# Optimization experiments

Hardware: AMD Instinct MI355X
Metric: run time of the kernel (lower is better)

## Reference

```python
import jax, jax.numpy as jnp
import numpy as np

B, CIN, COUT, N = 64, 1024, 1024, 49   # batch, in_features, out_features, flattened spatial
GROUPS = 1
CHUNK = 16                              # output-channel tile to bound intermediate memory


def setup_inputs() -> dict:
    key = jax.random.key(0)
    k1, k2 = jax.random.split(key)
    x = jax.random.normal(k1, (B, CIN, N), dtype=jnp.float32)
    weight = jax.random.normal(k2, (COUT, CIN // GROUPS), dtype=jnp.float32)  # std=1.0 init
    bias = jnp.zeros((COUT,), dtype=jnp.float32)
    return {"x": x, "weight": weight, "bias": bias}


def norm_dist_inf(x, weight, groups, chunk):
    # x: [B, Cin, N], weight: [Cout, Cin//groups]
    # out[b, o, n] = max_d |x[b, g(o)*d + d', n] - weight[o, d']|  (L-inf distance)
    Bb, Cin, Nn = x.shape
    Cout, d = weight.shape
    og = Cout // groups
    xg = x.reshape(Bb, groups, d, Nn)                 # [B, g, d, N]
    wg = weight.reshape(groups, og, d)                # [g, og, d]
    # tile output channels to avoid materializing [B, Cout, Cin, N]
    wchunks = wg.reshape(groups, og // chunk, chunk, d).transpose(1, 0, 2, 3)  # [nc, g, chunk, d]

    def body(carry, wc):
        # diff: [B, g, chunk, d, N] -> max over d
        out = jnp.max(jnp.abs(xg[:, :, None, :, :] - wc[None, :, :, :, None]), axis=3)
        return carry, out                              # [B, g, chunk, N]

    _, outs = jax.lax.scan(body, None, wchunks)        # [nc, B, g, chunk, N]
    out = outs.transpose(1, 2, 0, 3, 4).reshape(Bb, Cout, Nn)
    return out


def reference(x, weight, bias):
    out = norm_dist_inf(x, weight, GROUPS, CHUNK)      # [B, Cout, N]
    return out + bias[None, :, None]
```

## Files before the change

### kernel.cpp

```cpp
#include <hip/hip_runtime.h>


typedef float v2f  __attribute__((ext_vector_type(2)));
typedef float v4sf __attribute__((ext_vector_type(4)));

constexpr int CIN  = 1024;
constexpr int COUT = 1024;
constexpr int NN   = 49;
constexpr int P    = 3136;
constexpr int CPW  = 8;
constexpr int PIX  = 2;
constexpr int PT   = 64 * PIX;
constexpr int NPT  = (P + PT - 1) / PT;
constexpr int NTL  = CIN / 4;

#define PKSUB(d, wp, xp) \
    asm("v_pk_add_f32 %0, %1, %2 neg_lo:[0,1] neg_hi:[0,1]" \
        : "=v"(d) : "s"(wp), "v"(xp))
#define AMAX3(a, lo, hi) \
    asm("v_max3_f32 %0, %0, |%1|, |%2|" : "+v"(a) : "v"(lo), "v"(hi))

#define ISSUE_W(buf, ptr) do {                                               \
    asm volatile("s_load_dwordx4 %0, %1, 0x0"    : "=s"(buf[0]) : "s"(ptr)); \
    asm volatile("s_load_dwordx4 %0, %1, 0x1000" : "=s"(buf[1]) : "s"(ptr)); \
    asm volatile("s_load_dwordx4 %0, %1, 0x2000" : "=s"(buf[2]) : "s"(ptr)); \
    asm volatile("s_load_dwordx4 %0, %1, 0x3000" : "=s"(buf[3]) : "s"(ptr)); \
    asm volatile("s_load_dwordx4 %0, %1, 0x4000" : "=s"(buf[4]) : "s"(ptr)); \
    asm volatile("s_load_dwordx4 %0, %1, 0x5000" : "=s"(buf[5]) : "s"(ptr)); \
    asm volatile("s_load_dwordx4 %0, %1, 0x6000" : "=s"(buf[6]) : "s"(ptr)); \
    asm volatile("s_load_dwordx4 %0, %1, 0x7000" : "=s"(buf[7]) : "s"(ptr)); \
} while (0)

#define SDRAIN() asm volatile("s_waitcnt lgkmcnt(0)" ::: "memory")

__global__ __launch_bounds__(64) void ndist_kernel(
    const float* __restrict__ x, const float* __restrict__ w,
    const float* __restrict__ bias, float* __restrict__ out)
{
    const int lane  = threadIdx.x;
    const int o0    = blockIdx.x * CPW;
    const int pbase = blockIdx.y * PT;

    int bb[PIX], nn_[PIX];
    const float* xp[PIX];
#pragma unroll
    for (int i = 0; i < PIX; ++i) {
        const bool valid = (pbase + i * 64) < P;
        const int  pi    = (valid ? pbase + i * 64 : pbase) + lane;
        bb[i]  = pi / NN;
        nn_[i] = pi - bb[i] * NN;
        xp[i]  = x + (size_t)bb[i] * (CIN * NN) + nn_[i];
    }

    const float* wb = w + (size_t)o0 * CIN;

    float acc[CPW][PIX];
#pragma unroll
    for (int c = 0; c < CPW; ++c)
#pragma unroll
        for (int i = 0; i < PIX; ++i) acc[c][i] = 0.0f;

    v2f  xA[PIX][2], xB[PIX][2];
    v4sf wS0[8], wS1[8];

#define LOAD_X(dst, kt) do {                                   \
        _Pragma("unroll")                                      \
        for (int i = 0; i < PIX; ++i) {                        \
            float a0 = xp[i][((kt) * 4 + 0) * NN];             \
            float a1 = xp[i][((kt) * 4 + 1) * NN];             \
            float a2 = xp[i][((kt) * 4 + 2) * NN];             \
            float a3 = xp[i][((kt) * 4 + 3) * NN];             \
            dst[i][0] = (v2f){a0, a1};                         \
            dst[i][1] = (v2f){a2, a3};                         \
        }                                                      \
    } while (0)

#define COMPUTE(xv, wbuf) do {                                 \
        _Pragma("unroll")                                      \
        for (int c = 0; c < CPW; ++c) {                        \
            v2f wlo = __builtin_shufflevector(wbuf[c], wbuf[c], 0, 1); \
            v2f whi = __builtin_shufflevector(wbuf[c], wbuf[c], 2, 3); \
            _Pragma("unroll")                                  \
            for (int i = 0; i < PIX; ++i) {                    \
                v2f d0, d1;                                    \
                PKSUB(d0, wlo, xv[i][0]);                      \
                PKSUB(d1, whi, xv[i][1]);                      \
                AMAX3(acc[c][i], d0.x, d0.y);                  \
                AMAX3(acc[c][i], d1.x, d1.y);                  \
            }                                                  \
        }                                                      \
    } while (0)

    ISSUE_W(wS0, wb);
    LOAD_X(xA, 0);
    SDRAIN();

    for (int kt = 0; kt < NTL - 2; kt += 2) {
        const float* w1 = wb + (size_t)(kt + 1) * 4;
        ISSUE_W(wS1, w1);
        LOAD_X(xB, kt + 1);
        COMPUTE(xA, wS0);
        SDRAIN();

        const float* w2 = wb + (size_t)(kt + 2) * 4;
        ISSUE_W(wS0, w2);
        LOAD_X(xA, kt + 2);
        COMPUTE(xB, wS1);
        SDRAIN();
    }
    {
        const float* w1 = wb + (size_t)(NTL - 1) * 4;
        ISSUE_W(wS1, w1);
        LOAD_X(xB, NTL - 1);
        COMPUTE(xA, wS0);
        SDRAIN();
        COMPUTE(xB, wS1);
    }

#pragma unroll
    for (int i = 0; i < PIX; ++i) {
        if ((pbase + i * 64) < P) {
#pragma unroll
            for (int c = 0; c < CPW; ++c) {
                const int o = o0 + c;
                out[((size_t)bb[i] * COUT + o) * NN + nn_[i]] = acc[c][i] + bias[o];
            }
        }
    }
}

extern "C" void kernel_launch(void* const* d_in, const int* in_sizes, int n_in,
                              void* d_out, int out_size, void* d_ws, size_t ws_size,
                              hipStream_t stream) {
    const float* x    = (const float*)d_in[0];
    const float* w    = (const float*)d_in[1];
    const float* bias = (const float*)d_in[2];
    float* out        = (float*)d_out;

    dim3 grid(COUT / CPW, NPT);
    ndist_kernel<<<grid, 64, 0, stream>>>(x, w, bias, out);
}
```

Baseline: 154.5 us.

## Pre-transpose x to channel-major workspace and load adjacent pixel pairs

```diff
diff --git a/kernel.cpp b/kernel.cpp
--- a/kernel.cpp
+++ b/kernel.cpp
@@ -9,16 +9,21 @@
 constexpr int NN   = 49;
 constexpr int P    = 3136;
 constexpr int CPW  = 8;
-constexpr int PIX  = 2;
-constexpr int PT   = 64 * PIX;
-constexpr int NPT  = (P + PT - 1) / PT;
+constexpr int PT   = 128;
+constexpr int NPT  = 25;
 constexpr int NTL  = CIN / 4;
 
+#define PKBC_LO(d, wp, xp) \
+    asm("v_pk_add_f32 %0, %1, %2 op_sel:[0,0] op_sel_hi:[0,1] neg_lo:[1,0] neg_hi:[1,0]" \
+        : "=v"(d) : "s"(wp), "v"(xp))
+#define PKBC_HI(d, wp, xp) \
+    asm("v_pk_add_f32 %0, %1, %2 op_sel:[1,0] op_sel_hi:[1,1] neg_lo:[1,0] neg_hi:[1,0]" \
+        : "=v"(d) : "s"(wp), "v"(xp))
+#define AMAX3(a, lo, hi) \
+    asm("v_max3_f32 %0, %0, |%1|, |%2|" : "+v"(a) : "v"(lo), "v"(hi))
 #define PKSUB(d, wp, xp) \
     asm("v_pk_add_f32 %0, %1, %2 neg_lo:[0,1] neg_hi:[0,1]" \
         : "=v"(d) : "s"(wp), "v"(xp))
-#define AMAX3(a, lo, hi) \
-    asm("v_max3_f32 %0, %0, |%1|, |%2|" : "+v"(a) : "v"(lo), "v"(hi))
 
 #define ISSUE_W(buf, ptr) do {                                               \
     asm volatile("s_load_dwordx4 %0, %1, 0x0"    : "=s"(buf[0]) : "s"(ptr)); \
@@ -30,64 +35,57 @@
     asm volatile("s_load_dwordx4 %0, %1, 0x6000" : "=s"(buf[6]) : "s"(ptr)); \
     asm volatile("s_load_dwordx4 %0, %1, 0x7000" : "=s"(buf[7]) : "s"(ptr)); \
 } while (0)
+#define SDRAIN() do { asm volatile("s_waitcnt lgkmcnt(0)" ::: "memory"); \
+                      __builtin_amdgcn_sched_barrier(0); } while (0)
 
-#define SDRAIN() asm volatile("s_waitcnt lgkmcnt(0)" ::: "memory")
+__global__ void transpose_x(const float* __restrict__ x, float* __restrict__ xT) {
+    const int pp = threadIdx.x & 63, kk = threadIdx.x >> 6;
+    const int p = blockIdx.x * 64 + pp;
+    const int k = blockIdx.y * 4 + kk;
+    const int b = p / NN, n = p - b * NN;
+    xT[(size_t)k * P + p] = x[(size_t)b * (CIN * NN) + (size_t)k * NN + n];
+}
 
 __global__ __launch_bounds__(64) void ndist_kernel(
-    const float* __restrict__ x, const float* __restrict__ w,
+    const float* __restrict__ xT, const float* __restrict__ w,
     const float* __restrict__ bias, float* __restrict__ out)
 {
     const int lane  = threadIdx.x;
     const int o0    = blockIdx.x * CPW;
     const int pbase = blockIdx.y * PT;
+    const int p0    = pbase + 2 * lane;
+    const int pc    = (p0 <= P - 2) ? p0 : (P - 2);
 
-    int bb[PIX], nn_[PIX];
-    const float* xp[PIX];
-#pragma unroll
-    for (int i = 0; i < PIX; ++i) {
-        const bool valid = (pbase + i * 64) < P;
-        const int  pi    = (valid ? pbase + i * 64 : pbase) + lane;
-        bb[i]  = pi / NN;
-        nn_[i] = pi - bb[i] * NN;
-        xp[i]  = x + (size_t)bb[i] * (CIN * NN) + nn_[i];
-    }
-
+    const float* __restrict__ xb = xT + pc;
     const float* wb = w + (size_t)o0 * CIN;
 
-    float acc[CPW][PIX];
+    float acc[CPW][2];
 #pragma unroll
-    for (int c = 0; c < CPW; ++c)
-#pragma unroll
-        for (int i = 0; i < PIX; ++i) acc[c][i] = 0.0f;
+    for (int c = 0; c < CPW; ++c) { acc[c][0] = 0.0f; acc[c][1] = 0.0f; }
 
-    v2f  xA[PIX][2], xB[PIX][2];
+    v2f  xA[4], xB[4];
     v4sf wS0[8], wS1[8];
 
 #define LOAD_X(dst, kt) do {                                   \
         _Pragma("unroll")                                      \
-        for (int i = 0; i < PIX; ++i) {                        \
-            float a0 = xp[i][((kt) * 4 + 0) * NN];             \
-            float a1 = xp[i][((kt) * 4 + 1) * NN];             \
-            float a2 = xp[i][((kt) * 4 + 2) * NN];             \
-            float a3 = xp[i][((kt) * 4 + 3) * NN];             \
-            dst[i][0] = (v2f){a0, a1};                         \
-            dst[i][1] = (v2f){a2, a3};                         \
-        }                                                      \
+        for (int j = 0; j < 4; ++j)                            \
+            dst[j] = *(const v2f*)(xb + (size_t)((kt) * 4 + j) * P); \
     } while (0)
 
 #define COMPUTE(xv, wbuf) do {                                 \
         _Pragma("unroll")                                      \
         for (int c = 0; c < CPW; ++c) {                        \
-            v2f wlo = __builtin_shufflevector(wbuf[c], wbuf[c], 0, 1); \
-            v2f whi = __builtin_shufflevector(wbuf[c], wbuf[c], 2, 3); \
-            _Pragma("unroll")                                  \
-            for (int i = 0; i < PIX; ++i) {                    \
-                v2f d0, d1;                                    \
-                PKSUB(d0, wlo, xv[i][0]);                      \
-                PKSUB(d1, whi, xv[i][1]);                      \
-                AMAX3(acc[c][i], d0.x, d0.y);                  \
-                AMAX3(acc[c][i], d1.x, d1.y);                  \
-            }                                                  \
+            v2f p01 = __builtin_shufflevector(wbuf[c], wbuf[c], 0, 1); \
+            v2f p23 = __builtin_shufflevector(wbuf[c], wbuf[c], 2, 3); \
+            v2f d0, d1, d2, d3;                                \
+            PKBC_LO(d0, p01, xv[0]);                           \
+            PKBC_HI(d1, p01, xv[1]);                           \
+            AMAX3(acc[c][0], d0.x, d1.x);                      \
+            AMAX3(acc[c][1], d0.y, d1.y);                      \
+            PKBC_LO(d2, p23, xv[2]);                           \
+            PKBC_HI(d3, p23, xv[3]);                           \
+            AMAX3(acc[c][0], d2.x, d3.x);                      \
+            AMAX3(acc[c][1], d2.y, d3.y);                      \
         }                                                      \
     } while (0)
 
@@ -96,21 +94,18 @@
     SDRAIN();
 
     for (int kt = 0; kt < NTL - 2; kt += 2) {
-        const float* w1 = wb + (size_t)(kt + 1) * 4;
-        ISSUE_W(wS1, w1);
+        ISSUE_W(wS1, wb + (size_t)(kt + 1) * 4);
         LOAD_X(xB, kt + 1);
         COMPUTE(xA, wS0);
         SDRAIN();
 
-        const float* w2 = wb + (size_t)(kt + 2) * 4;
-        ISSUE_W(wS0, w2);
+        ISSUE_W(wS0, wb + (size_t)(kt + 2) * 4);
         LOAD_X(xA, kt + 2);
         COMPUTE(xB, wS1);
         SDRAIN();
     }
     {
-        const float* w1 = wb + (size_t)(NTL - 1) * 4;
-        ISSUE_W(wS1, w1);
+        ISSUE_W(wS1, wb + (size_t)(NTL - 1) * 4);
         LOAD_X(xB, NTL - 1);
         COMPUTE(xA, wS0);
         SDRAIN();
@@ -118,14 +113,55 @@
     }
 
 #pragma unroll
-    for (int i = 0; i < PIX; ++i) {
-        if ((pbase + i * 64) < P) {
+    for (int c = 0; c < CPW; ++c) {
+        const int o = o0 + c;
+        const float bv = bias[o];
 #pragma unroll
-            for (int c = 0; c < CPW; ++c) {
-                const int o = o0 + c;
-                out[((size_t)bb[i] * COUT + o) * NN + nn_[i]] = acc[c][i] + bias[o];
+        for (int i = 0; i < 2; ++i) {
+            const int px = p0 + i;
+            if (px < P) {
+                const int b = px / NN, n = px - b * NN;
+                out[((size_t)b * COUT + o) * NN + n] = acc[c][i] + bv;
             }
         }
+    }
+}
+
+__global__ __launch_bounds__(128) void ndist_fallback(
+    const float* __restrict__ x, const float* __restrict__ w,
+    const float* __restrict__ bias, float* __restrict__ out)
+{
+    const int lane = threadIdx.x & 63;
+    const int wid  = __builtin_amdgcn_readfirstlane(threadIdx.x >> 6);
+    const int p = blockIdx.y * 64 + lane;
+    const int b = p / NN, n = p - b * NN;
+    const int o0 = blockIdx.x * 16 + wid * 8;
+    const float* __restrict__ xrow = x + (size_t)b * CIN * NN + n;
+    const float* __restrict__ wb   = w + (size_t)o0 * CIN;
+
+    float acc[8];
+#pragma unroll
+    for (int c = 0; c < 8; ++c) acc[c] = 0.0f;
+
+    for (int kt = 0; kt < NTL; ++kt) {
+        v2f xv0 = { xrow[(kt * 4 + 0) * NN], xrow[(kt * 4 + 1) * NN] };
+        v2f xv1 = { xrow[(kt * 4 + 2) * NN], xrow[(kt * 4 + 3) * NN] };
+#pragma unroll
+        for (int c = 0; c < 8; ++c) {
+            v4sf t = *(const v4sf*)(wb + (size_t)c * CIN + kt * 4);
+            v2f lo = __builtin_shufflevector(t, t, 0, 1);
+            v2f hi = __builtin_shufflevector(t, t, 2, 3);
+            v2f d0, d1;
+            PKSUB(d0, lo, xv0);
+            PKSUB(d1, hi, xv1);
+            AMAX3(acc[c], d0.x, d0.y);
+            AMAX3(acc[c], d1.x, d1.y);
+        }
+    }
+#pragma unroll
+    for (int c = 0; c < 8; ++c) {
+        const int o = o0 + c;
+        out[((size_t)b * COUT + o) * NN + n] = acc[c] + bias[o];
     }
 }
 
@@ -137,6 +173,12 @@
     const float* bias = (const float*)d_in[2];
     float* out        = (float*)d_out;
 
-    dim3 grid(COUT / CPW, NPT);
-    ndist_kernel<<<grid, 64, 0, stream>>>(x, w, bias, out);
+    const size_t xt_bytes = (size_t)CIN * P * sizeof(float);
+    if (ws_size >= xt_bytes) {
+        float* xT = (float*)d_ws;
+        transpose_x<<<dim3(49, 256), 256, 0, stream>>>(x, xT);
+        ndist_kernel<<<dim3(COUT / CPW, NPT), 64, 0, stream>>>(xT, w, bias, out);
+    } else {
+        ndist_fallback<<<dim3(COUT / 16, 49), 128, 0, stream>>>(x, w, bias, out);
+    }
 }
```

After: 173.2 us. 12.1% more time.
